# Optimization experiments

Hardware: AMD Instinct MI355X
Metric: run time of the kernel (lower is better)

The kernel has to match this reference:

```python
import jax, jax.numpy as jnp
import numpy as np

B, L, D, H = 4, 2048, 1024, 16
DH = D // H  # 64
MASK_VALUE = -1000000.0
EPS = 1e-12


def setup_inputs() -> dict:
    key = jax.random.key(0)
    ks = jax.random.split(key, 7)
    s = 1.0 / np.sqrt(D)
    x = jax.random.normal(ks[0], (B, L, D), dtype=jnp.float32)
    Wq = jax.random.uniform(ks[1], (D, H * DH), jnp.float32, -s, s)
    Wk = jax.random.uniform(ks[2], (D, H * DH), jnp.float32, -s, s)
    Wv = jax.random.uniform(ks[3], (D, H * DH), jnp.float32, -s, s)
    Wo = jax.random.uniform(ks[4], (H * DH, D), jnp.float32, -s, s)
    gamma = jnp.ones((D,), jnp.float32)
    beta = jnp.zeros((D,), jnp.float32)
    # causal mask: True positions are masked (query m cannot attend to key n > m)
    attn_mask = jnp.triu(jnp.ones((L, L), dtype=bool), k=1)
    return {"x": x, "Wq": Wq, "Wk": Wk, "Wv": Wv, "Wo": Wo,
            "gamma": gamma, "beta": beta, "attn_mask": attn_mask}


def _layernorm(y, gamma, beta):
    mu = jnp.mean(y, axis=-1, keepdims=True)
    var = jnp.mean(jnp.square(y - mu), axis=-1, keepdims=True)
    return (y - mu) * jax.lax.rsqrt(var + EPS) * gamma + beta


def reference(x, Wq, Wk, Wv, Wo, gamma, beta, attn_mask):
    scale = 1.0 / np.sqrt(DH)
    # projections, reshape to heads: B L (H D) -> B H L D
    q = (x @ Wq).reshape(B, L, H, DH).transpose(0, 2, 1, 3)
    k = (x @ Wk).reshape(B, L, H, DH).transpose(0, 2, 1, 3)
    v = (x @ Wv).reshape(B, L, H, DH).transpose(0, 2, 1, 3)
    scores = jnp.einsum('bhmd,bhnd->bhmn', q, k) * scale
    scores = jnp.where(attn_mask, MASK_VALUE, scores)
    probs = jax.nn.softmax(scores, axis=-1)
    z = jnp.einsum('bhmn,bhnd->bhmd', probs, v)
    z = z.transpose(0, 2, 1, 3).reshape(B, L, H * DH)
    out = jax.nn.relu(z @ Wo)
    return _layernorm(out + x, gamma, beta)
```

## Files before the change

kernel.cpp:

```cpp
#include <hip/hip_runtime.h>
#include <math.h>

#define B_ 4
#define L_ 2048
#define D_ 1024
#define H_ 16
#define DH_ 64
#define QKV_N 3072

typedef unsigned short ushort_t;
typedef unsigned int uint_t;
using bf16x8 = __attribute__((ext_vector_type(8))) short;
using f32x4  = __attribute__((ext_vector_type(4))) float;

__device__ __forceinline__ ushort_t f2bf(float f) {
    union { float f; unsigned int u; } v; v.f = f;
    unsigned int u = v.u;
    unsigned int rnd = ((u >> 16) & 1u) + 0x7fffu;
    return (ushort_t)((u + rnd) >> 16);
}

__device__ __forceinline__ float bf2f(ushort_t u) {
    union { unsigned int u; float f; } v;
    v.u = ((unsigned int)u) << 16;
    return v.f;
}

__device__ __forceinline__ void glds16(const void* g, void* l) {
    __builtin_amdgcn_global_load_lds(
        (const __attribute__((address_space(1))) unsigned int*)g,
        (__attribute__((address_space(3))) unsigned int*)l, 16, 0, 0);
}

__global__ __launch_bounds__(256) void prep(const float* __restrict__ Wq,
                                            const float* __restrict__ Wk,
                                            const float* __restrict__ Wv,
                                            const float* __restrict__ Wo,
                                            const float* __restrict__ x,
                                            ushort_t* __restrict__ wcat,
                                            ushort_t* __restrict__ wto,
                                            ushort_t* __restrict__ xb) {
    const int t = threadIdx.x;
    if (blockIdx.z == 4) {
        const int bid = blockIdx.y * 16 + blockIdx.x;
        const int base = bid * 32768 + t * 4;
        #pragma unroll
        for (int it = 0; it < 32; ++it) {
            float4 v = *(const float4*)(x + base + it * 1024);
            ushort4 o;
            o.x = f2bf(v.x); o.y = f2bf(v.y); o.z = f2bf(v.z); o.w = f2bf(v.w);
            *(ushort4*)(xb + base + it * 1024) = o;
        }
        return;
    }
    __shared__ ushort_t tile[64][65];
    const int widx = blockIdx.z;
    const float* W = (widx == 0) ? Wq : (widx == 1) ? Wk : (widx == 2) ? Wv : Wo;
    ushort_t* dst = (widx < 3) ? (wcat + (size_t)widx * 1024 * 1024) : wto;
    const int j = t & 63, i0 = t >> 6;
    const int kbase = blockIdx.y * 64, nbase = blockIdx.x * 64;
    #pragma unroll
    for (int it = 0; it < 16; ++it) {
        int i = it * 4 + i0;
        tile[i][j] = f2bf(W[(size_t)(kbase + i) * 1024 + nbase + j]);
    }
    __syncthreads();
    #pragma unroll
    for (int it = 0; it < 16; ++it) {
        int nn = it * 4 + i0;
        dst[(size_t)(nbase + nn) * 1024 + kbase + j] = tile[j][nn];
    }
}

__global__ __launch_bounds__(256) void gemm_mfma(const ushort_t* __restrict__ A,
                                                 const ushort_t* __restrict__ Wt,
                                                 ushort_t* __restrict__ Cbf,
                                                 const ushort_t* __restrict__ resid,
                                                 ushort_t* __restrict__ vt,
                                                 int M, int N, int K, int fuse) {
    __shared__ ushort_t As[128 * 64];
    __shared__ ushort_t Bs[128 * 64];
    const int t = threadIdx.x;
    const int w = t >> 6, ln = t & 63;
    const int l15 = ln & 15, quad = ln >> 4;
    const int bm = blockIdx.y * 128, bn = blockIdx.x * 128;
    const int wm = (w & 1) * 64, wn = (w >> 1) * 64;

    const ushort_t* Ap[4];
    const ushort_t* Bp[4];
    #pragma unroll
    for (int j = 0; j < 4; ++j) {
        const int i = t + j * 256;
        const int r = i >> 3;
        const int qg = (i & 7) ^ (r & 7);
        Ap[j] = A  + (size_t)(bm + r) * K + qg * 8;
        Bp[j] = Wt + (size_t)(bn + r) * K + qg * 8;
    }

    f32x4 acc[4][4] = {};

    for (int k0 = 0; k0 < K; k0 += 64) {
        __syncthreads();
        #pragma unroll
        for (int j = 0; j < 4; ++j) {
            glds16(Ap[j] + k0, &As[(t + j * 256) * 8]);
            glds16(Bp[j] + k0, &Bs[(t + j * 256) * 8]);
        }
        __syncthreads();

        #pragma unroll
        for (int kw = 0; kw < 2; ++kw) {
            bf16x8 af[4], bfr[4];
            #pragma unroll
            for (int im = 0; im < 4; ++im) {
                int row = wm + im * 16 + l15;
                int phys = (kw * 4 + quad) ^ (row & 7);
                af[im] = *(const bf16x8*)&As[row * 64 + phys * 8];
            }
            #pragma unroll
            for (int in = 0; in < 4; ++in) {
                int row = wn + in * 16 + l15;
                int phys = (kw * 4 + quad) ^ (row & 7);
                bfr[in] = *(const bf16x8*)&Bs[row * 64 + phys * 8];
            }
            #pragma unroll
            for (int im = 0; im < 4; ++im)
                #pragma unroll
                for (int in = 0; in < 4; ++in)
                    acc[im][in] = __builtin_amdgcn_mfma_f32_16x16x32_bf16(
                        af[im], bfr[in], acc[im][in], 0, 0, 0);
        }
    }

    if (vt && bn >= 2048) {
        #pragma unroll
        for (int im = 0; im < 4; ++im) {
            #pragma unroll
            for (int in = 0; in < 4; ++in) {
                #pragma unroll
                for (int reg = 0; reg < 4; ++reg) {
                    int row = bm + wm + im * 16 + quad * 4 + reg;
                    int col = bn + wn + in * 16 + l15 - 2048;
                    int bb = row >> 11, tok = row & 2047;
                    int h = col >> 6, d = col & 63;
                    int tg = tok & 63;
                    int sc = (tg & 15) * 4 + (tg >> 4);
                    size_t addr = ((size_t)((bb * 16 + h) * 64 + d) << 11)
                                + (tok & ~63) + sc;
                    vt[addr] = f2bf(acc[im][in][reg]);
                }
            }
        }
    } else {
        #pragma unroll
        for (int im = 0; im < 4; ++im) {
            #pragma unroll
            for (int in = 0; in < 4; ++in) {
                #pragma unroll
                for (int reg = 0; reg < 4; ++reg) {
                    int row = bm + wm + im * 16 + quad * 4 + reg;
                    int col = bn + wn + in * 16 + l15;
                    size_t idx = (size_t)row * N + col;
                    float v = acc[im][in][reg];
                    if (fuse) v = fmaxf(v, 0.f) + bf2f(resid[idx]);
                    Cbf[idx] = f2bf(v);
                }
            }
        }
    }
}

__global__ __launch_bounds__(256) void attn_mfma(const ushort_t* __restrict__ qkv,
                                                 const ushort_t* __restrict__ Vt,
                                                 ushort_t* __restrict__ Zb) {
    __shared__ ushort_t Ks[128 * 64];
    __shared__ ushort_t Vs[64 * 128];
    __shared__ ushort_t Ps[4][32 * 72];
    const int t = threadIdx.x, w = t >> 6, ln = t & 63;
    const int l15 = ln & 15, quad = ln >> 4;
    const int bh = blockIdx.x;
    const int b = bh >> 4, h = bh & 15;
    const int Qt = 15 - blockIdx.y;

    bf16x8 ones;
    #pragma unroll
    for (int i = 0; i < 8; ++i) ones[i] = (short)0x3f80;

    int kkey[4], kq[4], vd[4], vcq[4];
    #pragma unroll
    for (int j = 0; j < 4; ++j) {
        int i = t + j * 256;
        kkey[j] = i >> 3;
        kq[j]   = (i & 7) ^ (kkey[j] & 7);
        vd[j]   = i >> 4;
        int cqp = i & 15;
        vcq[j]  = (cqp & 8) | ((cqp & 7) ^ (vd[j] & 7));
    }
    const ushort_t* Kgb = qkv + 1024 + (size_t)b * L_ * QKV_N + h * DH_;
    const ushort_t* Vgb = Vt + (size_t)((b * H_ + h) * DH_) * L_;

    bf16x8 qf[2][2];
    #pragma unroll
    for (int mt = 0; mt < 2; ++mt) {
        const ushort_t* qrow =
            qkv + (size_t)(b * L_ + Qt * 128 + w * 32 + mt * 16 + l15) * QKV_N + h * DH_;
        qf[mt][0] = *(const bf16x8*)(qrow + quad * 8);
        qf[mt][1] = *(const bf16x8*)(qrow + 32 + quad * 8);
    }

    f32x4 acc_o[2][4] = {};
    f32x4 l_acc[2] = {};

    const float c2 = 0.18033688f;

    for (int kt = 0; kt <= Qt; ++kt) {
        __syncthreads();
        #pragma unroll
        for (int j = 0; j < 4; ++j) {
            glds16(Kgb + (size_t)(kt * 128 + kkey[j]) * QKV_N + kq[j] * 8,
                   &Ks[(t + j * 256) * 8]);
            glds16(Vgb + (size_t)vd[j] * L_ + kt * 128 + vcq[j] * 8,
                   &Vs[(t + j * 256) * 8]);
        }
        __syncthreads();

        const bool masked = (kt == Qt);

        #pragma unroll
        for (int ph = 0; ph < 2; ++ph) {
            if (masked && ph && w < 2) continue;

            f32x4 acc_s[2][4] = {};
            __builtin_amdgcn_s_setprio(1);
            #pragma unroll
            for (int in = 0; in < 4; ++in) {
                const int key = ph * 64 + in * 16 + l15;
                #pragma unroll
                for (int ks = 0; ks < 2; ++ks) {
                    int phys = (ks * 4 + quad) ^ (key & 7);
                    bf16x8 kf = *(const bf16x8*)&Ks[key * 64 + phys * 8];
                    acc_s[0][in] = __builtin_amdgcn_mfma_f32_16x16x32_bf16(
                        qf[0][ks], kf, acc_s[0][in], 0, 0, 0);
                    acc_s[1][in] = __builtin_amdgcn_mfma_f32_16x16x32_bf16(
                        qf[1][ks], kf, acc_s[1][in], 0, 0, 0);
                }
            }
            __builtin_amdgcn_s_setprio(0);

            #pragma unroll
            for (int mt = 0; mt < 2; ++mt) {
                #pragma unroll
                for (int reg = 0; reg < 4; ++reg) {
                    const int row = mt * 16 + quad * 4 + reg;
                    float pv[4];
                    #pragma unroll
                    for (int in = 0; in < 4; ++in) {
                        float s2 = fmaf(acc_s[mt][in][reg], c2, -2.0f);
                        if (masked) {
                            int col = kt * 128 + ph * 64 + in * 16 + l15;
                            int qg  = Qt * 128 + w * 32 + row;
                            s2 = (col > qg) ? -100000.0f : s2;
                        }
                        pv[in] = __builtin_amdgcn_exp2f(s2);
                    }
                    uint_t u01 = __builtin_amdgcn_perm(
                        __float_as_uint(pv[1]), __float_as_uint(pv[0]), 0x07060302u);
                    uint_t u23 = __builtin_amdgcn_perm(
                        __float_as_uint(pv[3]), __float_as_uint(pv[2]), 0x07060302u);
                    uint2* dst = (uint2*)&Ps[w][row * 72 + l15 * 4];
                    *dst = make_uint2(u01, u23);
                }
            }

            __builtin_amdgcn_s_setprio(1);
            #pragma unroll
            for (int ks = 0; ks < 2; ++ks) {
                bf16x8 pf0 = *(const bf16x8*)&Ps[w][(l15) * 72 + ks * 32 + quad * 8];
                bf16x8 pf1 = *(const bf16x8*)&Ps[w][(16 + l15) * 72 + ks * 32 + quad * 8];
                #pragma unroll
                for (int in = 0; in < 4; ++in) {
                    const int d = in * 16 + l15;
                    int physv = ph * 8 + (((ks * 4 + quad) ^ (d & 7)));
                    bf16x8 vf = *(const bf16x8*)&Vs[d * 128 + physv * 8];
                    acc_o[0][in] = __builtin_amdgcn_mfma_f32_16x16x32_bf16(
                        vf, pf0, acc_o[0][in], 0, 0, 0);
                    acc_o[1][in] = __builtin_amdgcn_mfma_f32_16x16x32_bf16(
                        vf, pf1, acc_o[1][in], 0, 0, 0);
                }
                l_acc[0] = __builtin_amdgcn_mfma_f32_16x16x32_bf16(ones, pf0, l_acc[0], 0, 0, 0);
                l_acc[1] = __builtin_amdgcn_mfma_f32_16x16x32_bf16(ones, pf1, l_acc[1], 0, 0, 0);
            }
            __builtin_amdgcn_s_setprio(0);
        }
    }

    #pragma unroll
    for (int mt = 0; mt < 2; ++mt) {
        const float inv = 1.0f / l_acc[mt][0];
        const int row = b * L_ + Qt * 128 + w * 32 + mt * 16 + l15;
        #pragma unroll
        for (int in = 0; in < 4; ++in) {
            const int dbase = h * DH_ + in * 16 + quad * 4;
            f32x4 a = acc_o[mt][in];
            ushort4 o;
            o.x = f2bf(a[0] * inv); o.y = f2bf(a[1] * inv);
            o.z = f2bf(a[2] * inv); o.w = f2bf(a[3] * inv);
            *(ushort4*)(Zb + (size_t)row * D_ + dbase) = o;
        }
    }
}

__global__ __launch_bounds__(64) void ln_kernel(const ushort_t* __restrict__ Y,
                                                const float* __restrict__ gamma,
                                                const float* __restrict__ beta,
                                                float* __restrict__ out) {
    const int row = blockIdx.x;
    const int t = threadIdx.x;
    const ushort_t* y = Y + (size_t)row * D_;

    float v[16];
    #pragma unroll
    for (int s = 0; s < 4; ++s) {
        ushort4 u = *(const ushort4*)(y + s * 256 + t * 4);
        v[s * 4 + 0] = bf2f(u.x);
        v[s * 4 + 1] = bf2f(u.y);
        v[s * 4 + 2] = bf2f(u.z);
        v[s * 4 + 3] = bf2f(u.w);
    }

    float sum = 0.f;
    #pragma unroll
    for (int i = 0; i < 16; ++i) sum += v[i];
    #pragma unroll
    for (int k = 1; k < 64; k <<= 1) sum += __shfl_xor(sum, k, 64);
    const float mu = sum * (1.f / (float)D_);

    float var = 0.f;
    #pragma unroll
    for (int i = 0; i < 16; ++i) {
        float d = v[i] - mu;
        var += d * d;
    }
    #pragma unroll
    for (int k = 1; k < 64; k <<= 1) var += __shfl_xor(var, k, 64);
    const float rstd = rsqrtf(var * (1.f / (float)D_) + 1e-12f);

    #pragma unroll
    for (int s = 0; s < 4; ++s) {
        const int col = s * 256 + t * 4;
        float4 g  = *(const float4*)(gamma + col);
        float4 bb = *(const float4*)(beta + col);
        float4 o;
        o.x = (v[s * 4 + 0] - mu) * rstd * g.x + bb.x;
        o.y = (v[s * 4 + 1] - mu) * rstd * g.y + bb.y;
        o.z = (v[s * 4 + 2] - mu) * rstd * g.z + bb.z;
        o.w = (v[s * 4 + 3] - mu) * rstd * g.w + bb.w;
        *(float4*)(out + (size_t)row * D_ + col) = o;
    }
}

extern "C" void kernel_launch(void* const* d_in, const int* in_sizes, int n_in,
                              void* d_out, int out_size, void* d_ws, size_t ws_size,
                              hipStream_t stream) {
    const float* x     = (const float*)d_in[0];
    const float* Wq    = (const float*)d_in[1];
    const float* Wk    = (const float*)d_in[2];
    const float* Wv    = (const float*)d_in[3];
    const float* Wo    = (const float*)d_in[4];
    const float* gamma = (const float*)d_in[5];
    const float* beta  = (const float*)d_in[6];
    float* out = (float*)d_out;

    char* ws = (char*)d_ws;
    ushort_t* x_bf = (ushort_t*)(ws);
    ushort_t* wcat = (ushort_t*)(ws + (16u  << 20));
    ushort_t* wto  = (ushort_t*)(ws + (22u  << 20));
    ushort_t* qkv  = (ushort_t*)(ws + (24u  << 20));
    ushort_t* vt   = (ushort_t*)(ws + (72u  << 20));
    ushort_t* z_bf = (ushort_t*)(ws + (88u  << 20));
    ushort_t* y_bf = (ushort_t*)(ws + (104u << 20));

    const int M = B_ * L_;

    prep<<<dim3(16, 16, 5), 256, 0, stream>>>(Wq, Wk, Wv, Wo, x, wcat, wto, x_bf);

    gemm_mfma<<<dim3(QKV_N / 128, M / 128), 256, 0, stream>>>(
        x_bf, wcat, qkv, nullptr, vt, M, QKV_N, D_, 0);

    attn_mfma<<<dim3(B_ * H_, 16), 256, 0, stream>>>(qkv, vt, z_bf);

    gemm_mfma<<<dim3(D_ / 128, M / 128), 256, 0, stream>>>(
        z_bf, wto, y_bf, x_bf, nullptr, M, D_, D_, 1);

    ln_kernel<<<M, 64, 0, stream>>>(y_bf, gamma, beta, out);
}
```

Baseline: 277.4 us.

## Rewrite GEMM as 8-wave 256x128 tile with double-buffered LDS pipeline

Replaces the 4-wave 128x128 GEMM with a 512-thread kernel computing 256x128 tiles. Global-to-LDS loads are double-buffered in half-K chunks, with explicit vmcnt waits and barriers so loads overlap MFMA work, and MFMA sections run at raised priority. It also remaps block IDs across XCDs to improve L2 locality. The cost is a larger LDS footprint (96KB) and fewer blocks per CU, and the hand-written waitcnt scheduling is fragile.

```diff
diff --git a/kernel.cpp b/kernel.cpp
--- a/kernel.cpp
+++ b/kernel.cpp
@@ -72,96 +72,145 @@
     }
 }
 
-__global__ __launch_bounds__(256) void gemm_mfma(const ushort_t* __restrict__ A,
-                                                 const ushort_t* __restrict__ Wt,
-                                                 ushort_t* __restrict__ Cbf,
-                                                 const ushort_t* __restrict__ resid,
-                                                 ushort_t* __restrict__ vt,
-                                                 int M, int N, int K, int fuse) {
-    __shared__ ushort_t As[128 * 64];
-    __shared__ ushort_t Bs[128 * 64];
+__global__ __launch_bounds__(512) void gemm8p(const ushort_t* __restrict__ A,
+                                              const ushort_t* __restrict__ Wt,
+                                              ushort_t* __restrict__ Cbf,
+                                              const ushort_t* __restrict__ resid,
+                                              ushort_t* __restrict__ vt,
+                                              int M, int N, int K, int fuse) {
+    __shared__ ushort_t lds[49152];
     const int t = threadIdx.x;
     const int w = t >> 6, ln = t & 63;
     const int l15 = ln & 15, quad = ln >> 4;
-    const int bm = blockIdx.y * 128, bn = blockIdx.x * 128;
-    const int wm = (w & 1) * 64, wn = (w >> 1) * 64;
-
-    const ushort_t* Ap[4];
-    const ushort_t* Bp[4];
-    #pragma unroll
-    for (int j = 0; j < 4; ++j) {
-        const int i = t + j * 256;
-        const int r = i >> 3;
-        const int qg = (i & 7) ^ (r & 7);
-        Ap[j] = A  + (size_t)(bm + r) * K + qg * 8;
-        Bp[j] = Wt + (size_t)(bn + r) * K + qg * 8;
-    }
+    const int wrow = w >> 1, wcol = w & 1;
+
+    int bx = blockIdx.x, by = blockIdx.y;
+    {
+        int nwg = gridDim.x * gridDim.y;
+        if ((nwg & 7) == 0) {
+            int flat = by * gridDim.x + bx;
+            int nid = (flat & 7) * (nwg >> 3) + (flat >> 3);
+            by = nid / gridDim.x;
+            bx = nid - by * gridDim.x;
+        }
+    }
+    const int bm = by * 256, bn = bx * 128;
+
+    const ushort_t* Agp[2];
+    const ushort_t* Bgp;
+    #pragma unroll
+    for (int j = 0; j < 2; ++j) {
+        int r = j * 128 + (t >> 2);
+        int c = (t & 3) ^ ((r >> 1) & 3);
+        Agp[j] = A + (size_t)(bm + r) * K + c * 8;
+    }
+    {
+        int r = t >> 2;
+        int c = (t & 3) ^ ((r >> 1) & 3);
+        Bgp = Wt + (size_t)(bn + r) * K + c * 8;
+    }
+
+    const int swz8 = (quad ^ ((l15 >> 1) & 3)) * 8;
+    int aoff[4], boff[4];
+    #pragma unroll
+    for (int mf = 0; mf < 4; ++mf)
+        aoff[mf] = (wrow * 64 + mf * 16 + l15) * 32 + swz8;
+    #pragma unroll
+    for (int nf = 0; nf < 4; ++nf)
+        boff[nf] = (wcol * 64 + nf * 16 + l15) * 32 + swz8;
 
     f32x4 acc[4][4] = {};
-
-    for (int k0 = 0; k0 < K; k0 += 64) {
-        __syncthreads();
-        #pragma unroll
-        for (int j = 0; j < 4; ++j) {
-            glds16(Ap[j] + k0, &As[(t + j * 256) * 8]);
-            glds16(Bp[j] + k0, &Bs[(t + j * 256) * 8]);
-        }
-        __syncthreads();
-
-        #pragma unroll
-        for (int kw = 0; kw < 2; ++kw) {
-            bf16x8 af[4], bfr[4];
+    const int NT = K >> 6;
+
+#define ABASE(BUF, KH) ((BUF) * 24576 + (KH) * 12288)
+#define BBASE(BUF, KH) (ABASE(BUF, KH) + 8192)
+
+#define STAGE(BUF, KH, KT) do {                                             \
+        glds16(Agp[0] + (KT) * 64 + (KH) * 32, &lds[ABASE(BUF, KH) + t * 8]);\
+        glds16(Agp[1] + (KT) * 64 + (KH) * 32,                              \
+               &lds[ABASE(BUF, KH) + 4096 + t * 8]);                        \
+        glds16(Bgp + (KT) * 64 + (KH) * 32, &lds[BBASE(BUF, KH) + t * 8]);  \
+    } while (0)
+
+#define VM3 asm volatile("s_waitcnt vmcnt(3)" ::: "memory")
+#define VM0 asm volatile("s_waitcnt vmcnt(0)" ::: "memory")
+#define NOVM ((void)0)
+
+#define PHASE(BUF, KH, STAGEC, VMW) do {                                    \
+        bf16x8 af_[4], bf_[4];                                              \
+        _Pragma("unroll")                                                   \
+        for (int m_ = 0; m_ < 4; ++m_)                                      \
+            af_[m_] = *(const bf16x8*)&lds[ABASE(BUF, KH) + aoff[m_]];      \
+        _Pragma("unroll")                                                   \
+        for (int n_ = 0; n_ < 4; ++n_)                                      \
+            bf_[n_] = *(const bf16x8*)&lds[BBASE(BUF, KH) + boff[n_]];      \
+        STAGEC;                                                             \
+        VMW;                                                                \
+        __builtin_amdgcn_s_barrier();                                       \
+        asm volatile("s_waitcnt lgkmcnt(0)" ::: "memory");                  \
+        __builtin_amdgcn_s_setprio(1);                                      \
+        _Pragma("unroll")                                                   \
+        for (int m_ = 0; m_ < 4; ++m_)                                      \
+            _Pragma("unroll")                                               \
+            for (int n_ = 0; n_ < 4; ++n_)                                  \
+                acc[m_][n_] = __builtin_amdgcn_mfma_f32_16x16x32_bf16(      \
+                    af_[m_], bf_[n_], acc[m_][n_], 0, 0, 0);                \
+        __builtin_amdgcn_s_setprio(0);                                      \
+        __builtin_amdgcn_s_barrier();                                       \
+    } while (0)
+
+    STAGE(0, 0, 0);
+    STAGE(0, 1, 0);
+    STAGE(1, 0, 1);
+    VM3;
+    __builtin_amdgcn_s_barrier();
+
+    for (int it = 0; it < (NT >> 1); ++it) {
+        const int kt1 = 2 * it + 1, kt2 = 2 * it + 2, kt3 = 2 * it + 3;
+        const bool g2 = kt2 < NT, g3 = kt3 < NT;
+        PHASE(0, 0, STAGE(1, 1, kt1), NOVM);
+        PHASE(0, 1, if (g2) STAGE(0, 0, kt2),
+              { if (g2) { VM3; } else { VM0; } });
+        PHASE(1, 0, if (g2) STAGE(0, 1, kt2), NOVM);
+        PHASE(1, 1, if (g3) STAGE(1, 0, kt3),
+              { if (g3) { VM3; } else { VM0; } });
+    }
+
+#undef PHASE
+#undef STAGE
+#undef ABASE
+#undef BBASE
+
+    if (vt && bn >= 2048) {
+        #pragma unroll
+        for (int mf = 0; mf < 4; ++mf) {
             #pragma unroll
-            for (int im = 0; im < 4; ++im) {
-                int row = wm + im * 16 + l15;
-                int phys = (kw * 4 + quad) ^ (row & 7);
-                af[im] = *(const bf16x8*)&As[row * 64 + phys * 8];
-            }
-            #pragma unroll
-            for (int in = 0; in < 4; ++in) {
-                int row = wn + in * 16 + l15;
-                int phys = (kw * 4 + quad) ^ (row & 7);
-                bfr[in] = *(const bf16x8*)&Bs[row * 64 + phys * 8];
-            }
-            #pragma unroll
-            for (int im = 0; im < 4; ++im)
-                #pragma unroll
-                for (int in = 0; in < 4; ++in)
-                    acc[im][in] = __builtin_amdgcn_mfma_f32_16x16x32_bf16(
-                        af[im], bfr[in], acc[im][in], 0, 0, 0);
-        }
-    }
-
-    if (vt && bn >= 2048) {
-        #pragma unroll
-        for (int im = 0; im < 4; ++im) {
-            #pragma unroll
-            for (int in = 0; in < 4; ++in) {
+            for (int nf = 0; nf < 4; ++nf) {
                 #pragma unroll
                 for (int reg = 0; reg < 4; ++reg) {
-                    int row = bm + wm + im * 16 + quad * 4 + reg;
-                    int col = bn + wn + in * 16 + l15 - 2048;
+                    int row = bm + wrow * 64 + mf * 16 + quad * 4 + reg;
+                    int col = bn + wcol * 64 + nf * 16 + l15 - 2048;
                     int bb = row >> 11, tok = row & 2047;
                     int h = col >> 6, d = col & 63;
                     int tg = tok & 63;
                     int sc = (tg & 15) * 4 + (tg >> 4);
                     size_t addr = ((size_t)((bb * 16 + h) * 64 + d) << 11)
                                 + (tok & ~63) + sc;
-                    vt[addr] = f2bf(acc[im][in][reg]);
+                    vt[addr] = f2bf(acc[mf][nf][reg]);
                 }
             }
         }
     } else {
         #pragma unroll
-        for (int im = 0; im < 4; ++im) {
+        for (int mf = 0; mf < 4; ++mf) {
             #pragma unroll
-            for (int in = 0; in < 4; ++in) {
+            for (int nf = 0; nf < 4; ++nf) {
                 #pragma unroll
                 for (int reg = 0; reg < 4; ++reg) {
-                    int row = bm + wm + im * 16 + quad * 4 + reg;
-                    int col = bn + wn + in * 16 + l15;
+                    int row = bm + wrow * 64 + mf * 16 + quad * 4 + reg;
+                    int col = bn + wcol * 64 + nf * 16 + l15;
                     size_t idx = (size_t)row * N + col;
-                    float v = acc[im][in][reg];
+                    float v = acc[mf][nf][reg];
                     if (fuse) v = fmaxf(v, 0.f) + bf2f(resid[idx]);
                     Cbf[idx] = f2bf(v);
                 }
@@ -384,12 +433,12 @@
 
     prep<<<dim3(16, 16, 5), 256, 0, stream>>>(Wq, Wk, Wv, Wo, x, wcat, wto, x_bf);
 
-    gemm_mfma<<<dim3(QKV_N / 128, M / 128), 256, 0, stream>>>(
+    gemm8p<<<dim3(QKV_N / 128, M / 256), 512, 0, stream>>>(
         x_bf, wcat, qkv, nullptr, vt, M, QKV_N, D_, 0);
 
     attn_mfma<<<dim3(B_ * H_, 16), 256, 0, stream>>>(qkv, vt, z_bf);
 
-    gemm_mfma<<<dim3(D_ / 128, M / 128), 256, 0, stream>>>(
+    gemm8p<<<dim3(D_ / 128, M / 256), 512, 0, stream>>>(
         z_bf, wto, y_bf, x_bf, nullptr, M, D_, D_, 1);
 
     ln_kernel<<<M, 64, 0, stream>>>(y_bf, gamma, beta, out);
```

Result: no change. 280.7 us (+1.2%).
